# Optimization experiments

Hardware: AMD Instinct MI355X
Metric: run time of the kernel (lower is better)

## Reference

```python
import jax, jax.numpy as jnp
import numpy as np

N_EDGES = 100000      # hyperedge table rows
N_INC = 2000000       # incidences (rows of hyper_node)
D_E = 64              # edge_in_channels
D_N = 64              # node_in_channels
D_OUT = 64            # node_out_channels


def setup_inputs() -> dict:
    key = jax.random.key(0)
    k1, k2, k3, k4 = jax.random.split(key, 4)
    hyperedge = jax.random.normal(k1, (N_EDGES, D_E), dtype=jnp.float32)
    hyper_node = jax.random.normal(k2, (N_INC, D_N), dtype=jnp.float32)
    ve_affiliation = jax.random.randint(k3, (2, N_INC), 0, N_EDGES, dtype=jnp.int64)
    # Linear weight stored torch-style [out, in]; xavier-ish scale
    W = jax.random.normal(k4, (D_OUT, D_E * 2 + D_N), dtype=jnp.float32) * 0.05
    b = jnp.zeros((D_OUT,), dtype=jnp.float32)
    return {"hyperedge": hyperedge, "hyper_node": hyper_node,
            "ve_affiliation": ve_affiliation, "W": W, "b": b}


def reference(hyperedge, hyper_node, ve_affiliation, W, b):
    # gather edge features for both endpoints of each incidence
    edge_i = hyperedge[ve_affiliation[0]]          # [N_INC, D_E]
    edge_j = hyperedge[ve_affiliation[1]]          # [N_INC, D_E]
    x = jnp.concatenate((edge_i, edge_j, hyper_node), axis=-1)  # [N_INC, 2*D_E+D_N]
    h = x @ W.T + b                                # [N_INC, D_OUT]
    return jax.nn.relu(h)
```

## Files before the change

### kernel.cpp

```cpp
#include <hip/hip_runtime.h>


typedef __bf16 bf16x8 __attribute__((ext_vector_type(8)));
typedef float  f32x4  __attribute__((ext_vector_type(4)));

static __device__ __forceinline__ bf16x8 cvt8(f32x4 a, f32x4 b) {
  bf16x8 r;
  r[0] = (__bf16)a[0]; r[1] = (__bf16)a[1]; r[2] = (__bf16)a[2]; r[3] = (__bf16)a[3];
  r[4] = (__bf16)b[0]; r[5] = (__bf16)b[1]; r[6] = (__bf16)b[2]; r[7] = (__bf16)b[3];
  return r;
}

static __device__ __forceinline__ bf16x8 load_frag(const float* __restrict__ p) {
  f32x4 a = *(const f32x4*)p;
  f32x4 b = *(const f32x4*)(p + 4);
  return cvt8(a, b);
}

#define N_INC    2000000
#define N_TILES  (N_INC / 16)

__global__ __launch_bounds__(256, 2) void e2v_mfma(
    const float* __restrict__ hyperedge,
    const float* __restrict__ hyper_node,
    const int*   __restrict__ aff,
    const float* __restrict__ W,
    const float* __restrict__ bias,
    float*       __restrict__ out)
{
  const int lane = threadIdx.x & 63;
  const int wid  = (blockIdx.x * blockDim.x + threadIdx.x) >> 6;
  const int nw   = (gridDim.x * blockDim.x) >> 6;
  const int m    = lane & 15;
  const int quad = lane >> 4;
  const int koff = quad * 8;

  bf16x8 Bf[4][6];
  #pragma unroll
  for (int t = 0; t < 4; ++t) {
    const float* wr = W + (t * 16 + m) * 192 + koff;
    #pragma unroll
    for (int f = 0; f < 6; ++f)
      Bf[t][f] = load_frag(wr + f * 32);
  }
  float bv[4];
  #pragma unroll
  for (int t = 0; t < 4; ++t) bv[t] = bias[t * 16 + m];

  const int* __restrict__ aff0 = aff;
  const int* __restrict__ aff1 = aff + N_INC;

  for (int tile = wid; tile < N_TILES; tile += nw) {
    const int n_base = tile * 16;
    const int i0 = aff0[n_base + m];
    const int i1 = aff1[n_base + m];
    const float* e0 = hyperedge  + (long)i0 * 64 + koff;
    const float* e1 = hyperedge  + (long)i1 * 64 + koff;
    const float* nd = hyper_node + (long)(n_base + m) * 64 + koff;

    bf16x8 A[6];
    A[0] = load_frag(e0);
    A[1] = load_frag(e0 + 32);
    A[2] = load_frag(e1);
    A[3] = load_frag(e1 + 32);
    A[4] = load_frag(nd);
    A[5] = load_frag(nd + 32);

    f32x4 acc[4] = { {0.f,0.f,0.f,0.f}, {0.f,0.f,0.f,0.f},
                     {0.f,0.f,0.f,0.f}, {0.f,0.f,0.f,0.f} };
    #pragma unroll
    for (int f = 0; f < 6; ++f) {
      #pragma unroll
      for (int t = 0; t < 4; ++t)
        acc[t] = __builtin_amdgcn_mfma_f32_16x16x32_bf16(A[f], Bf[t][f], acc[t], 0, 0, 0);
    }

    #pragma unroll
    for (int t = 0; t < 4; ++t) {
      const int o = t * 16 + m;
      #pragma unroll
      for (int r = 0; r < 4; ++r) {
        const int inc = n_base + quad * 4 + r;
        float v = acc[t][r] + bv[t];
        out[(long)inc * 64 + o] = v > 0.f ? v : 0.f;
      }
    }
  }
}

extern "C" void kernel_launch(void* const* d_in, const int* in_sizes, int n_in,
                              void* d_out, int out_size, void* d_ws, size_t ws_size,
                              hipStream_t stream) {
  const float* hyperedge  = (const float*)d_in[0];
  const float* hyper_node = (const float*)d_in[1];
  const int*   aff        = (const int*)d_in[2];
  const float* W          = (const float*)d_in[3];
  const float* bias       = (const float*)d_in[4];
  float* out = (float*)d_out;

  dim3 grid(4096), block(256);
  hipLaunchKernelGGL(e2v_mfma, grid, block, 0, stream,
                     hyperedge, hyper_node, aff, W, bias, out);
}
```

Baseline: 1.004 ms.

## Precompute per-edge projections then gather projected rows per incidence

Splits the linear layer algebraically. A first kernel projects each of the 100k hyperedge rows through both edge halves of W (with bias folded in) into a 128-wide workspace table. A second kernel gathers the two projected 64-float rows per incidence, adds the node-feature MFMA result, and applies ReLU, with prefetch of the next tile's indices and vectorized stores. This cuts MFMA work per incidence by two thirds and avoids converting gathered edge features, but it adds a second launch and relies on the workspace being large enough, otherwise it falls back to the old kernel.

```diff
diff --git a/kernel.cpp b/kernel.cpp
--- a/kernel.cpp
+++ b/kernel.cpp
@@ -17,8 +17,135 @@
   return cvt8(a, b);
 }
 
+#define N_EDGES  100000
 #define N_INC    2000000
 #define N_TILES  (N_INC / 16)
+#define E_TILES  (N_EDGES / 16)
+
+__global__ __launch_bounds__(256, 2) void edge_proj(
+    const float* __restrict__ hyperedge,
+    const float* __restrict__ W,
+    const float* __restrict__ bias,
+    float*       __restrict__ proj)
+{
+  const int lane = threadIdx.x & 63;
+  const int wid  = (blockIdx.x * blockDim.x + threadIdx.x) >> 6;
+  if (wid >= E_TILES) return;
+  const int m    = lane & 15;
+  const int quad = lane >> 4;
+  const int koff = quad * 8;
+
+  bf16x8 Wf[8][2];
+  #pragma unroll
+  for (int t = 0; t < 8; ++t) {
+    const float* wr = W + (long)((t & 3) * 16 + m) * 192 + (t >> 2) * 64 + koff;
+    #pragma unroll
+    for (int f = 0; f < 2; ++f)
+      Wf[t][f] = load_frag(wr + f * 32);
+  }
+
+  const int ebase = wid * 16;
+  const float* er = hyperedge + (long)(ebase + m) * 64 + koff;
+  bf16x8 hef0 = load_frag(er);
+  bf16x8 hef1 = load_frag(er + 32);
+
+  f32x4 acc[8] = { {0,0,0,0},{0,0,0,0},{0,0,0,0},{0,0,0,0},
+                   {0,0,0,0},{0,0,0,0},{0,0,0,0},{0,0,0,0} };
+  #pragma unroll
+  for (int t = 0; t < 8; ++t) {
+    acc[t] = __builtin_amdgcn_mfma_f32_16x16x32_bf16(Wf[t][0], hef0, acc[t], 0, 0, 0);
+    acc[t] = __builtin_amdgcn_mfma_f32_16x16x32_bf16(Wf[t][1], hef1, acc[t], 0, 0, 0);
+  }
+
+  float* pr = proj + (long)(ebase + m) * 128 + quad * 4;
+  #pragma unroll
+  for (int t = 0; t < 8; ++t) {
+    f32x4 v = acc[t];
+    if (t < 4) {
+      f32x4 bv = *(const f32x4*)(bias + t * 16 + quad * 4);
+      v[0] += bv[0]; v[1] += bv[1]; v[2] += bv[2]; v[3] += bv[3];
+    }
+    *(f32x4*)(pr + t * 16) = v;
+  }
+}
+
+__global__ __launch_bounds__(256, 4) void e2v_gather(
+    const float* __restrict__ hyper_node,
+    const int*   __restrict__ aff,
+    const float* __restrict__ W,
+    const float* __restrict__ proj,
+    float*       __restrict__ out)
+{
+  const int lane = threadIdx.x & 63;
+  const int wid  = (blockIdx.x * blockDim.x + threadIdx.x) >> 6;
+  const int nw   = (gridDim.x * blockDim.x) >> 6;
+  const int m    = lane & 15;
+  const int quad = lane >> 4;
+  const int koff = quad * 8;
+
+  bf16x8 Wf2[4][2];
+  #pragma unroll
+  for (int t = 0; t < 4; ++t) {
+    const float* wr = W + (long)(t * 16 + m) * 192 + 128 + koff;
+    #pragma unroll
+    for (int f = 0; f < 2; ++f)
+      Wf2[t][f] = load_frag(wr + f * 32);
+  }
+
+  const int* __restrict__ aff0 = aff;
+  const int* __restrict__ aff1 = aff + N_INC;
+
+  int tile = wid;
+  if (tile >= N_TILES) return;
+
+  int ni0 = aff0[tile * 16 + m];
+  int ni1 = aff1[tile * 16 + m];
+
+  for (; tile < N_TILES; tile += nw) {
+    const int i0 = ni0;
+    const int i1 = ni1;
+    const int nb = tile * 16;
+
+    const int nt = tile + nw;
+    if (nt < N_TILES) {
+      ni0 = aff0[nt * 16 + m];
+      ni1 = aff1[nt * 16 + m];
+    }
+
+    const float* p0 = proj + (long)i0 * 128 + quad * 4;
+    const float* p1 = proj + (long)i1 * 128 + 64 + quad * 4;
+    f32x4 g0[4], g1[4];
+    #pragma unroll
+    for (int t = 0; t < 4; ++t) {
+      g0[t] = *(const f32x4*)(p0 + t * 16);
+      g1[t] = *(const f32x4*)(p1 + t * 16);
+    }
+
+    const float* nd = hyper_node + (long)(nb + m) * 64 + koff;
+    bf16x8 Nf0 = load_frag(nd);
+    bf16x8 Nf1 = load_frag(nd + 32);
+
+    f32x4 acc[4] = { {0,0,0,0},{0,0,0,0},{0,0,0,0},{0,0,0,0} };
+    #pragma unroll
+    for (int t = 0; t < 4; ++t)
+      acc[t] = __builtin_amdgcn_mfma_f32_16x16x32_bf16(Wf2[t][0], Nf0, acc[t], 0, 0, 0);
+    #pragma unroll
+    for (int t = 0; t < 4; ++t)
+      acc[t] = __builtin_amdgcn_mfma_f32_16x16x32_bf16(Wf2[t][1], Nf1, acc[t], 0, 0, 0);
+
+    float* op = out + (long)(nb + m) * 64 + quad * 4;
+    #pragma unroll
+    for (int t = 0; t < 4; ++t) {
+      f32x4 v;
+      #pragma unroll
+      for (int r = 0; r < 4; ++r) {
+        float x = acc[t][r] + g0[t][r] + g1[t][r];
+        v[r] = x > 0.f ? x : 0.f;
+      }
+      *(f32x4*)(op + t * 16) = v;
+    }
+  }
+}
 
 __global__ __launch_bounds__(256, 2) void e2v_mfma(
     const float* __restrict__ hyperedge,
@@ -98,7 +225,15 @@
   const float* bias       = (const float*)d_in[4];
   float* out = (float*)d_out;
 
-  dim3 grid(4096), block(256);
-  hipLaunchKernelGGL(e2v_mfma, grid, block, 0, stream,
-                     hyperedge, hyper_node, aff, W, bias, out);
-}
+  const size_t need = (size_t)N_EDGES * 128 * sizeof(float);
+  if (ws_size >= need) {
+    float* proj = (float*)d_ws;
+    hipLaunchKernelGGL(edge_proj, dim3((E_TILES * 64 + 255) / 256), dim3(256), 0, stream,
+                       hyperedge, W, bias, proj);
+    hipLaunchKernelGGL(e2v_gather, dim3(4096), dim3(256), 0, stream,
+                       hyper_node, aff, W, proj, out);
+  } else {
+    hipLaunchKernelGGL(e2v_mfma, dim3(4096), dim3(256), 0, stream,
+                       hyperedge, hyper_node, aff, W, bias, out);
+  }
+}
```

After: 989.9 us. Within noise of the previous version (-1.4%).
